# Kernel tuning notes

Measured on AMD Instinct MI355X. Metric: run time of the kernel, lower is better.

Reference implementation:

```python
import jax, jax.numpy as jnp
import numpy as np

OUT_H, OUT_W = 736, 240  # hardcoded interpolate target in the module


def resize_bilinear_ac(x, out_h, out_w):
    # bilinear, align_corners=True, NCHW
    B, C, H, W = x.shape
    def lin(n_in, n_out):
        pos = jnp.arange(n_out, dtype=jnp.float32) * (float(n_in - 1) / float(n_out - 1))
        i0 = jnp.floor(pos).astype(jnp.int32)
        i1 = jnp.minimum(i0 + 1, n_in - 1)
        f = pos - i0.astype(jnp.float32)
        return i0, i1, f
    hi0, hi1, hf = lin(H, out_h)
    xh = (x[:, :, hi0, :] * (1.0 - hf)[None, None, :, None]
          + x[:, :, hi1, :] * hf[None, None, :, None])
    wi0, wi1, wf = lin(W, out_w)
    return xh[..., wi0] * (1.0 - wf) + xh[..., wi1] * wf


def setup_inputs() -> dict:
    key = jax.random.key(0)
    x = jax.random.normal(key, (32, 7, 368, 120), dtype=jnp.float32)
    w = np.ones((6, 1, 1, 2), dtype=np.float32)
    w[:, :, :, 1] = -1.0  # fixed [1, -1] horizontal edge filter, depthwise
    return {"x": x, "dw_weight": jnp.asarray(w)}


def reference(x, dw_weight):
    C = x.shape[1]
    xi = resize_bilinear_ac(x, OUT_H, OUT_W)              # [B,C,736,240]
    lab = jnp.argmax(xi, axis=1)                          # [B,736,240]
    lab = jnp.transpose(lab, (0, 2, 1))                   # [B,240,736]
    oh = jax.nn.one_hot(lab, C, axis=1, dtype=jnp.float32)  # [B,C,240,736]

    # --- out1: depthwise [1,-1] diff with right pad of 0.5, relu, flipped argmax ---
    d = oh[:, :C - 1]                                     # drop background channel
    padded = jnp.pad(d, ((0, 0), (0, 0), (0, 0), (0, 1)), constant_values=0.5)
    w0 = dw_weight[:, 0, 0, 0][None, :, None, None]
    w1 = dw_weight[:, 0, 0, 1][None, :, None, None]
    edge = jax.nn.relu(padded[..., :-1] * w0 + padded[..., 1:] * w1)  # [B,C-1,240,736]
    t = jnp.transpose(edge, (0, 3, 2, 1))                 # [B,736,240,C-1]
    t = jnp.flip(t, axis=1)
    out1 = jnp.argmax(t, axis=1, keepdims=True)           # [B,1,240,C-1] int

    # --- out2: background channel summed over 8 bands of 30 rows ---
    xr = oh[:, -1]                                        # [B,240,736]
    B = xr.shape[0]
    out2 = xr.reshape(B, 8, 30, OUT_H).sum(axis=(2, 3)).reshape(B, 1, 8)
    return out1, out2
```

## Files before the change

kernel.cpp:

```cpp
#include <hip/hip_runtime.h>
#include <hip/hip_bf16.h>
#include <float.h>

#define BB 32
#define CC 7
#define IH 368
#define IW 120
#define OH 736
#define OW 240
#define NCH 46
#define CHROWS 16

#define OUT1_ELEMS (BB * OW * 6)

__global__ __launch_bounds__(256) void fused_label_edge_kernel(
    const float* __restrict__ x, unsigned long long* __restrict__ part) {
  int blk = blockIdx.x;
  int b = blk / NCH;
  int k = blk % NCH;
  int w = threadIdx.x;
  if (w >= OW) return;

  const float RH = (float)(367.0 / 735.0);
  const float RW = (float)(119.0 / 239.0);

  float pw = __fmul_rn((float)w, RW);
  int wi0 = (int)floorf(pw);
  int wi1 = min(wi0 + 1, IW - 1);
  float wf = __fsub_rn(pw, (float)wi0);
  float omwf = __fsub_rn(1.0f, wf);

  int h0 = k * CHROWS;
  int nrows = min(CHROWS + 1, OH - h0);

  const float* xb = x + (size_t)b * CC * IH * IW;

  float t00[CC], t01[CC], t10[CC], t11[CC];
  int cur = -2;

  unsigned e0 = 0, e1 = 0, e2 = 0, e3 = 0, e4 = 0, e5 = 0;
  int c6 = 0;
  int prev = -1;

  for (int hl = 0; hl < nrows; ++hl) {
    int h = h0 + hl;
    float ph = __fmul_rn((float)h, RH);
    int hi0 = (int)floorf(ph);
    float hf = __fsub_rn(ph, (float)hi0);
    float omhf = __fsub_rn(1.0f, hf);
    int hi1 = min(hi0 + 1, IH - 1);

    if (hi0 == cur + 1) {
#pragma unroll
      for (int c = 0; c < CC; ++c) {
        t00[c] = t10[c];
        t01[c] = t11[c];
        const float* rp = xb + c * (IH * IW) + hi1 * IW;
        t10[c] = rp[wi0];
        t11[c] = rp[wi1];
      }
      cur = hi0;
    } else if (hi0 != cur) {
#pragma unroll
      for (int c = 0; c < CC; ++c) {
        const float* r0 = xb + c * (IH * IW) + hi0 * IW;
        const float* r1 = xb + c * (IH * IW) + hi1 * IW;
        t00[c] = r0[wi0];
        t01[c] = r0[wi1];
        t10[c] = r1[wi0];
        t11[c] = r1[wi1];
      }
      cur = hi0;
    }

    float best = -FLT_MAX;
    int bc = 0;
#pragma unroll
    for (int c = 0; c < CC; ++c) {
      float va = __fadd_rn(__fmul_rn(t00[c], omhf), __fmul_rn(t10[c], hf));
      float vb = __fadd_rn(__fmul_rn(t01[c], omhf), __fmul_rn(t11[c], hf));
      float v = __fadd_rn(__fmul_rn(va, omwf), __fmul_rn(vb, wf));
      if (v > best) { best = v; bc = c; }
    }

    if (hl < CHROWS) c6 += (bc == 6);
    if (hl > 0 && bc != prev) {
      e0 = (prev == 0) ? (unsigned)hl : e0;
      e1 = (prev == 1) ? (unsigned)hl : e1;
      e2 = (prev == 2) ? (unsigned)hl : e2;
      e3 = (prev == 3) ? (unsigned)hl : e3;
      e4 = (prev == 4) ? (unsigned)hl : e4;
      e5 = (prev == 5) ? (unsigned)hl : e5;
    }
    prev = bc;
  }

  unsigned long long u =
      (unsigned long long)e0 | ((unsigned long long)e1 << 8) |
      ((unsigned long long)e2 << 16) | ((unsigned long long)e3 << 24) |
      ((unsigned long long)e4 << 32) | ((unsigned long long)e5 << 40) |
      ((unsigned long long)(unsigned)c6 << 48);
  part[(size_t)(b * NCH + k) * OW + w] = u;
}

__global__ __launch_bounds__(256) void finalize_kernel(
    const unsigned long long* __restrict__ part, float* __restrict__ out) {
  int b = blockIdx.x;
  int w = threadIdx.x;

  __shared__ int cnt[256];

  int c6 = 0;
  if (w < OW) {
    int g0 = -1, g1 = -1, g2 = -1, g3 = -1, g4 = -1, g5 = -1;
    const unsigned long long* P = part + (size_t)b * NCH * OW + w;
#pragma unroll
    for (int k = 0; k < NCH; ++k) {
      unsigned long long u = P[(size_t)k * OW];
      int base = k * CHROWS - 1;
      unsigned v;
      v = (unsigned)(u) & 0xffu;        if (v) g0 = base + (int)v;
      v = (unsigned)(u >> 8) & 0xffu;   if (v) g1 = base + (int)v;
      v = (unsigned)(u >> 16) & 0xffu;  if (v) g2 = base + (int)v;
      v = (unsigned)(u >> 24) & 0xffu;  if (v) g3 = base + (int)v;
      v = (unsigned)(u >> 32) & 0xffu;  if (v) g4 = base + (int)v;
      v = (unsigned)(u >> 40) & 0xffu;  if (v) g5 = base + (int)v;
      c6 += (int)((u >> 48) & 0xffu);
    }
    float* o1 = out + (size_t)b * (OW * 6) + w * 6;
    o1[0] = (g0 >= 0) ? (float)(735 - g0) : 0.0f;
    o1[1] = (g1 >= 0) ? (float)(735 - g1) : 0.0f;
    o1[2] = (g2 >= 0) ? (float)(735 - g2) : 0.0f;
    o1[3] = (g3 >= 0) ? (float)(735 - g3) : 0.0f;
    o1[4] = (g4 >= 0) ? (float)(735 - g4) : 0.0f;
    o1[5] = (g5 >= 0) ? (float)(735 - g5) : 0.0f;
  }

  cnt[threadIdx.x] = (w < OW) ? c6 : 0;
  __syncthreads();
  if (threadIdx.x < 8) {
    int s = 0;
#pragma unroll
    for (int i = 0; i < 30; ++i) s += cnt[threadIdx.x * 30 + i];
    out[OUT1_ELEMS + b * 8 + threadIdx.x] = (float)s;
  }
}

extern "C" void kernel_launch(void* const* d_in, const int* in_sizes, int n_in,
                              void* d_out, int out_size, void* d_ws, size_t ws_size,
                              hipStream_t stream) {
  const float* x = (const float*)d_in[0];
  float* out = (float*)d_out;
  unsigned long long* part = (unsigned long long*)d_ws;

  fused_label_edge_kernel<<<BB * NCH, 256, 0, stream>>>(x, part);
  finalize_kernel<<<BB, 256, 0, stream>>>(part, out);
}
```

Baseline: 100.1 us.

## Fuse finalize into main kernel via last-block atomic counter; prefetch next input row

```diff
diff --git a/kernel.cpp b/kernel.cpp
--- a/kernel.cpp
+++ b/kernel.cpp
@@ -13,111 +13,122 @@
 
 #define OUT1_ELEMS (BB * OW * 6)
 
-__global__ __launch_bounds__(256) void fused_label_edge_kernel(
-    const float* __restrict__ x, unsigned long long* __restrict__ part) {
+#define PART_ELEMS (BB * NCH * OW)
+#define CNT_OFF    ((size_t)PART_ELEMS * 8)
+
+__global__ __launch_bounds__(256) void fused_all_kernel(
+    const float* __restrict__ x, unsigned long long* __restrict__ part,
+    int* __restrict__ counters, float* __restrict__ out) {
   int blk = blockIdx.x;
   int b = blk / NCH;
   int k = blk % NCH;
   int w = threadIdx.x;
-  if (w >= OW) return;
+  bool active = (w < OW);
 
   const float RH = (float)(367.0 / 735.0);
   const float RW = (float)(119.0 / 239.0);
 
-  float pw = __fmul_rn((float)w, RW);
-  int wi0 = (int)floorf(pw);
-  int wi1 = min(wi0 + 1, IW - 1);
-  float wf = __fsub_rn(pw, (float)wi0);
-  float omwf = __fsub_rn(1.0f, wf);
+  if (active) {
+    float pw = __fmul_rn((float)w, RW);
+    int wi0 = (int)floorf(pw);
+    int wi1 = min(wi0 + 1, IW - 1);
+    float wf = __fsub_rn(pw, (float)wi0);
+    float omwf = __fsub_rn(1.0f, wf);
 
-  int h0 = k * CHROWS;
-  int nrows = min(CHROWS + 1, OH - h0);
+    int h0 = k * CHROWS;
+    int nrows = min(CHROWS + 1, OH - h0);
 
-  const float* xb = x + (size_t)b * CC * IH * IW;
+    const float* xb = x + (size_t)b * CC * IH * IW;
 
-  float t00[CC], t01[CC], t10[CC], t11[CC];
-  int cur = -2;
+    float ph0 = __fmul_rn((float)h0, RH);
+    int cur = (int)floorf(ph0);
+    int rB = min(cur + 1, IH - 1);
+    int rP = min(cur + 2, IH - 1);
+    float tA0[CC], tA1[CC], tB0[CC], tB1[CC], tP0[CC], tP1[CC];
+#pragma unroll
+    for (int c = 0; c < CC; ++c) {
+      const float* pa = xb + c * (IH * IW) + cur * IW;
+      const float* pb = xb + c * (IH * IW) + rB * IW;
+      const float* pp = xb + c * (IH * IW) + rP * IW;
+      tA0[c] = pa[wi0]; tA1[c] = pa[wi1];
+      tB0[c] = pb[wi0]; tB1[c] = pb[wi1];
+      tP0[c] = pp[wi0]; tP1[c] = pp[wi1];
+    }
 
-  unsigned e0 = 0, e1 = 0, e2 = 0, e3 = 0, e4 = 0, e5 = 0;
-  int c6 = 0;
-  int prev = -1;
+    unsigned e0 = 0, e1 = 0, e2 = 0, e3 = 0, e4 = 0, e5 = 0;
+    int c6 = 0;
+    int prev = -1;
 
-  for (int hl = 0; hl < nrows; ++hl) {
-    int h = h0 + hl;
-    float ph = __fmul_rn((float)h, RH);
-    int hi0 = (int)floorf(ph);
-    float hf = __fsub_rn(ph, (float)hi0);
-    float omhf = __fsub_rn(1.0f, hf);
-    int hi1 = min(hi0 + 1, IH - 1);
+    for (int hl = 0; hl < nrows; ++hl) {
+      int h = h0 + hl;
+      float ph = __fmul_rn((float)h, RH);
+      int hi0 = (int)floorf(ph);
+      float hf = __fsub_rn(ph, (float)hi0);
+      float omhf = __fsub_rn(1.0f, hf);
 
-    if (hi0 == cur + 1) {
+      if (hi0 != cur) {
+        cur = hi0;
+        int rN = min(cur + 2, IH - 1);
+#pragma unroll
+        for (int c = 0; c < CC; ++c) {
+          tA0[c] = tB0[c]; tA1[c] = tB1[c];
+          tB0[c] = tP0[c]; tB1[c] = tP1[c];
+          const float* pp = xb + c * (IH * IW) + rN * IW;
+          tP0[c] = pp[wi0];
+          tP1[c] = pp[wi1];
+        }
+      }
+
+      float best = -FLT_MAX;
+      int bc = 0;
 #pragma unroll
       for (int c = 0; c < CC; ++c) {
-        t00[c] = t10[c];
-        t01[c] = t11[c];
-        const float* rp = xb + c * (IH * IW) + hi1 * IW;
-        t10[c] = rp[wi0];
-        t11[c] = rp[wi1];
+        float va = __fadd_rn(__fmul_rn(tA0[c], omhf), __fmul_rn(tB0[c], hf));
+        float vb = __fadd_rn(__fmul_rn(tA1[c], omhf), __fmul_rn(tB1[c], hf));
+        float v  = __fadd_rn(__fmul_rn(va, omwf), __fmul_rn(vb, wf));
+        if (v > best) { best = v; bc = c; }
       }
-      cur = hi0;
-    } else if (hi0 != cur) {
-#pragma unroll
-      for (int c = 0; c < CC; ++c) {
-        const float* r0 = xb + c * (IH * IW) + hi0 * IW;
-        const float* r1 = xb + c * (IH * IW) + hi1 * IW;
-        t00[c] = r0[wi0];
-        t01[c] = r0[wi1];
-        t10[c] = r1[wi0];
-        t11[c] = r1[wi1];
+
+      if (hl < CHROWS) c6 += (bc == 6);
+      if (hl > 0 && bc != prev) {
+        e0 = (prev == 0) ? (unsigned)hl : e0;
+        e1 = (prev == 1) ? (unsigned)hl : e1;
+        e2 = (prev == 2) ? (unsigned)hl : e2;
+        e3 = (prev == 3) ? (unsigned)hl : e3;
+        e4 = (prev == 4) ? (unsigned)hl : e4;
+        e5 = (prev == 5) ? (unsigned)hl : e5;
       }
-      cur = hi0;
+      prev = bc;
     }
 
-    float best = -FLT_MAX;
-    int bc = 0;
-#pragma unroll
-    for (int c = 0; c < CC; ++c) {
-      float va = __fadd_rn(__fmul_rn(t00[c], omhf), __fmul_rn(t10[c], hf));
-      float vb = __fadd_rn(__fmul_rn(t01[c], omhf), __fmul_rn(t11[c], hf));
-      float v = __fadd_rn(__fmul_rn(va, omwf), __fmul_rn(vb, wf));
-      if (v > best) { best = v; bc = c; }
-    }
-
-    if (hl < CHROWS) c6 += (bc == 6);
-    if (hl > 0 && bc != prev) {
-      e0 = (prev == 0) ? (unsigned)hl : e0;
-      e1 = (prev == 1) ? (unsigned)hl : e1;
-      e2 = (prev == 2) ? (unsigned)hl : e2;
-      e3 = (prev == 3) ? (unsigned)hl : e3;
-      e4 = (prev == 4) ? (unsigned)hl : e4;
-      e5 = (prev == 5) ? (unsigned)hl : e5;
-    }
-    prev = bc;
+    unsigned long long u =
+        (unsigned long long)e0 | ((unsigned long long)e1 << 8) |
+        ((unsigned long long)e2 << 16) | ((unsigned long long)e3 << 24) |
+        ((unsigned long long)e4 << 32) | ((unsigned long long)e5 << 40) |
+        ((unsigned long long)(unsigned)c6 << 48);
+    part[(size_t)(b * NCH + k) * OW + w] = u;
   }
 
-  unsigned long long u =
-      (unsigned long long)e0 | ((unsigned long long)e1 << 8) |
-      ((unsigned long long)e2 << 16) | ((unsigned long long)e3 << 24) |
-      ((unsigned long long)e4 << 32) | ((unsigned long long)e5 << 40) |
-      ((unsigned long long)(unsigned)c6 << 48);
-  part[(size_t)(b * NCH + k) * OW + w] = u;
-}
-
-__global__ __launch_bounds__(256) void finalize_kernel(
-    const unsigned long long* __restrict__ part, float* __restrict__ out) {
-  int b = blockIdx.x;
-  int w = threadIdx.x;
+  __threadfence();
+  __syncthreads();
+  __shared__ int sflag;
+  if (threadIdx.x == 0) {
+    int old = atomicAdd(&counters[b], 1);
+    sflag = (old == NCH - 1) ? 1 : 0;
+  }
+  __syncthreads();
+  if (!sflag) return;
+  __threadfence();
 
   __shared__ int cnt[256];
-
-  int c6 = 0;
-  if (w < OW) {
+  int c6t = 0;
+  if (active) {
     int g0 = -1, g1 = -1, g2 = -1, g3 = -1, g4 = -1, g5 = -1;
     const unsigned long long* P = part + (size_t)b * NCH * OW + w;
 #pragma unroll
-    for (int k = 0; k < NCH; ++k) {
-      unsigned long long u = P[(size_t)k * OW];
-      int base = k * CHROWS - 1;
+    for (int kk = 0; kk < NCH; ++kk) {
+      unsigned long long u = P[(size_t)kk * OW];
+      int base = kk * CHROWS - 1;
       unsigned v;
       v = (unsigned)(u) & 0xffu;        if (v) g0 = base + (int)v;
       v = (unsigned)(u >> 8) & 0xffu;   if (v) g1 = base + (int)v;
@@ -125,7 +136,7 @@
       v = (unsigned)(u >> 24) & 0xffu;  if (v) g3 = base + (int)v;
       v = (unsigned)(u >> 32) & 0xffu;  if (v) g4 = base + (int)v;
       v = (unsigned)(u >> 40) & 0xffu;  if (v) g5 = base + (int)v;
-      c6 += (int)((u >> 48) & 0xffu);
+      c6t += (int)((u >> 48) & 0xffu);
     }
     float* o1 = out + (size_t)b * (OW * 6) + w * 6;
     o1[0] = (g0 >= 0) ? (float)(735 - g0) : 0.0f;
@@ -136,7 +147,7 @@
     o1[5] = (g5 >= 0) ? (float)(735 - g5) : 0.0f;
   }
 
-  cnt[threadIdx.x] = (w < OW) ? c6 : 0;
+  cnt[threadIdx.x] = active ? c6t : 0;
   __syncthreads();
   if (threadIdx.x < 8) {
     int s = 0;
@@ -152,7 +163,8 @@
   const float* x = (const float*)d_in[0];
   float* out = (float*)d_out;
   unsigned long long* part = (unsigned long long*)d_ws;
+  int* counters = (int*)((char*)d_ws + CNT_OFF);
 
-  fused_label_edge_kernel<<<BB * NCH, 256, 0, stream>>>(x, part);
-  finalize_kernel<<<BB, 256, 0, stream>>>(part, out);
+  hipMemsetAsync(counters, 0, BB * sizeof(int), stream);
+  fused_all_kernel<<<BB * NCH, 256, 0, stream>>>(x, part, counters, out);
 }
```

Result: slower. 247.7 us (+147.3%).
